# Kernel optimization log

Hardware: AMD Instinct MI355X
Metric: run time of the kernel (lower is better)

Reference implementation:

```python
import jax, jax.numpy as jnp
import numpy as np
from jax import lax

T, B, D, H, L = 256, 64, 512, 1024, 2


def _lstm_params(key):
    k = 1.0 / np.sqrt(H)
    params = {}
    in_dims = [D] + [H] * (L - 1)
    for l in range(L):
        key, k1, k2, k3, k4 = jax.random.split(key, 5)
        params[f"W_ih{l}"] = jax.random.uniform(k1, (4 * H, in_dims[l]), jnp.float32, -k, k)
        params[f"W_hh{l}"] = jax.random.uniform(k2, (4 * H, H), jnp.float32, -k, k)
        params[f"b_ih{l}"] = jax.random.uniform(k3, (4 * H,), jnp.float32, -k, k)
        params[f"b_hh{l}"] = jax.random.uniform(k4, (4 * H,), jnp.float32, -k, k)
    return params


def setup_inputs() -> dict:
    key = jax.random.key(0)
    k_in, k_rst, k_p = jax.random.split(key, 3)
    inp = {
        "input": jax.random.normal(k_in, (T, B, D), jnp.float32),
        "reset": jax.random.randint(k_rst, (T, B), 0, 2, jnp.int32),
        "h0": jnp.zeros((B, L, H), jnp.float32),
        "c0": jnp.zeros((B, L, H), jnp.float32),
    }
    inp.update(_lstm_params(k_p))
    return inp


def _run(input, reset_f, h0, c0, Wi, Wh, bi, bh):
    # state: [L, B, H]
    h = jnp.transpose(h0, (1, 0, 2))
    c = jnp.transpose(c0, (1, 0, 2))

    def step(carry, xt):
        h, c = carry
        x_t, r_t = xt  # x_t: [B, D], r_t: [B]
        keep = (1.0 - r_t)[None, :, None]  # reset gate zeroes state where reset==1
        h = h * keep
        c = c * keep
        x = x_t
        hs, cs = [], []
        for l in range(L):
            # gate order in torch nn.LSTM: i, f, g, o
            gates = x @ Wi[l].T + bi[l] + h[l] @ Wh[l].T + bh[l]
            i_g, f_g, g_g, o_g = jnp.split(gates, 4, axis=-1)
            c_new = jax.nn.sigmoid(f_g) * c[l] + jax.nn.sigmoid(i_g) * jnp.tanh(g_g)
            h_new = jax.nn.sigmoid(o_g) * jnp.tanh(c_new)
            hs.append(h_new)
            cs.append(c_new)
            x = h_new
        return (jnp.stack(hs), jnp.stack(cs)), x

    (h, c), outputs = lax.scan(step, (h, c), (input, reset_f))
    # back to [B, L, H] as in the torch module's returned state
    return outputs, jnp.transpose(h, (1, 0, 2)), jnp.transpose(c, (1, 0, 2))


def reference(input, reset, h0, c0, W_ih0, W_hh0, b_ih0, b_hh0, W_ih1, W_hh1, b_ih1, b_hh1):
    reset_f = reset.astype(jnp.float32)
    Wi = [W_ih0, W_ih1]
    Wh = [W_hh0, W_hh1]
    bi = [b_ih0, b_ih1]
    bh = [b_hh0, b_hh1]
    outputs, hN, cN = _run(input, reset_f, h0, c0, Wi, Wh, bi, bh)
    return outputs, (hN, cN)
```

## Files before the change

### kernel.cpp

```cpp
#include <hip/hip_runtime.h>

typedef __bf16 bf16x8 __attribute__((ext_vector_type(8)));
typedef float f32x4 __attribute__((ext_vector_type(4)));
typedef unsigned u32x4 __attribute__((ext_vector_type(4)));
typedef unsigned short u16;

constexpr int T = 256, B = 64, D = 512, H = 1024;
constexpr int G4 = 4 * H;
constexpr int NBLK = 256;
constexpr int NTHR = 256;
constexpr int BS = 32;
constexpr int MT = 2;

__device__ __forceinline__ u16 f2bf(float f) {
  unsigned u = __builtin_bit_cast(unsigned, f);
  u += 0x7fffu + ((u >> 16) & 1u);
  return (u16)(u >> 16);
}

__device__ __forceinline__ f32x4 mfma16(bf16x8 a, bf16x8 b, f32x4 c) {
  return __builtin_amdgcn_mfma_f32_16x16x32_bf16(a, b, c, 0, 0, 0);
}

__device__ __forceinline__ float sigm(float x) { return 1.f / (1.f + expf(-x)); }

__device__ __forceinline__ int ldflag(const int* f, int i) {
  return __hip_atomic_load(&f[i], __ATOMIC_RELAXED, __HIP_MEMORY_SCOPE_AGENT);
}

__global__ void cvt_bf16(const float* __restrict__ src, u16* __restrict__ dst, int n4) {
  int i = blockIdx.x * blockDim.x + threadIdx.x;
  int st = gridDim.x * blockDim.x;
  for (; i < n4; i += st) {
    float4 v = reinterpret_cast<const float4*>(src)[i];
    ushort4 o;
    o.x = f2bf(v.x); o.y = f2bf(v.y); o.z = f2bf(v.z); o.w = f2bf(v.w);
    reinterpret_cast<ushort4*>(dst)[i] = o;
  }
}

__global__ void init_state(const float* __restrict__ h0,
                           u16* __restrict__ xs1, u16* __restrict__ h1buf,
                           const float* __restrict__ bih0, const float* __restrict__ bhh0,
                           const float* __restrict__ bih1, const float* __restrict__ bhh1,
                           float* __restrict__ bias0, float* __restrict__ bias1,
                           int* __restrict__ flags) {
  int i = blockIdx.x * blockDim.x + threadIdx.x;
  if (i < NBLK) flags[i] = 0;
  if (i < 2 * B * H) {
    int l = i / (B * H), rem = i % (B * H);
    int b = rem / H, k = rem % H;
    u16 v = f2bf(h0[(size_t)b * 2 * H + (size_t)l * H + k]);
    if (l == 0) xs1[(size_t)b * H + k] = v;
    else        h1buf[(size_t)b * H + k] = v;
  }
  if (i < G4) {
    bias0[i] = bih0[i] + bhh0[i];
    bias1[i] = bih1[i] + bhh1[i];
  }
}

template <int L>
__device__ __forceinline__ void run_layer(
    const u16* __restrict__ xin, const u16* __restrict__ wx, const u16* __restrict__ wh,
    const float* __restrict__ bias, u16* __restrict__ xs1, u16* __restrict__ h1b,
    const float* __restrict__ c0, const int* __restrict__ reset,
    float* __restrict__ out, int* __restrict__ flags, int half, int col0, int lb,
    f32x4* __restrict__ red, unsigned* __restrict__ rbits, float* __restrict__ lbias,
    const int s1mask, const int h1mask, const int full) {
  constexpr int KX   = L ? H : D;
  constexpr int NCX  = KX / 32;
  constexpr int NCXW = NCX / 4;
  constexpr int NHW  = (H / 32) / 4;
  constexpr int NCW  = NCXW + NHW;
  const size_t BH = (size_t)B * H;
  const size_t OUT_HN = (size_t)T * BH;
  const size_t OUT_CN = OUT_HN + 2 * BH;

  const int tid  = threadIdx.x;
  const int ks   = tid >> 6;
  const int lane = tid & 63;
  const int q    = lane >> 4;
  const int ln   = lane & 15;

  for (int t = tid; t < T; t += NTHR) {
    unsigned v = 0;
#pragma unroll 8
    for (int i = 0; i < 32; ++i)
      v |= (unsigned)(reset[t * B + half * BS + i] & 1) << i;
    rbits[t] = v;
  }
  if (tid < 64) lbias[tid] = bias[(tid >> 4) * H + col0 + (tid & 15)];

  u32x4 wreg[4][NCW];
#pragma unroll
  for (int g = 0; g < 4; ++g)
#pragma unroll
    for (int cc = 0; cc < NCW; ++cc) {
      const bool isx = cc < NCXW;
      const int c = isx ? ks * NCXW + cc : ks * NHW + (cc - NCXW);
      const u16* W = isx ? wx : wh;
      const int stride = isx ? KX : H;
      const int kk = c * 32 + q * 8;
      wreg[g][cc] = *reinterpret_cast<const u32x4*>(
          W + (size_t)(g * H + col0 + ln) * stride + kk);
    }
#pragma unroll
  for (int g = 0; g < 4; ++g)
#pragma unroll
    for (int cc = 0; cc < NCW; ++cc)
      asm volatile("" : "+a"(wreg[g][cc]));

  const int b0l = (tid >> 4) * 4;
  const int cl  = col0 + (tid & 15);
  float creg[4] = {0.f, 0.f, 0.f, 0.f};
  if (tid < 128)
#pragma unroll
    for (int r = 0; r < 4; ++r)
      creg[r] = c0[(size_t)(half * BS + b0l + r) * 2 * H + (size_t)L * H + cl];

  __syncthreads();
  float bval[4];
#pragma unroll
  for (int g = 0; g < 4; ++g) bval[g] = lbias[g * 16 + (tid & 15)];

  float hv[4] = {0.f, 0.f, 0.f, 0.f};

  uint4 xf[NCXW][MT];
  auto load_xfrags = [&](const u16* xsrc) {
#pragma unroll
    for (int cc = 0; cc < NCXW; ++cc) {
      const int kk = (ks * NCXW + cc) * 32 + q * 8;
#pragma unroll
      for (int m = 0; m < MT; ++m)
        xf[cc][m] = *reinterpret_cast<const uint4*>(
            xsrc + (size_t)(half * BS + 16 * m + ln) * KX + kk);
    }
  };
  if (full && L == 0) load_xfrags(xin);

  const int gbase = (L * 2 + half) * 64 + ks * 16;
  const int xbase = half * 64 + ks * 16;
  int l0seen = 0;

  for (int s = 0; s <= T; ++s) {
    const bool active = (L == 0) ? (s < T) : (s >= 1);
    const int t = (L == 0) ? s : s - 1;
    if (active) {
      const u16* hsrc = (L == 0) ? xs1 + (size_t)(s & s1mask) * BH
                                 : h1b + (size_t)(t & h1mask) * BH;
      if (full) {
        while (ldflag(flags, gbase + (lane & 15)) < s) __builtin_amdgcn_s_sleep(1);
        asm volatile("" ::: "memory");
      } else {
        for (;;) {
          int a = ldflag(flags, lane),       b = ldflag(flags, 64 + lane);
          int c = ldflag(flags, 128 + lane), d = ldflag(flags, 192 + lane);
          int m1 = a < b ? a : b, m2 = c < d ? c : d;
          if ((m1 < m2 ? m1 : m2) >= s) break;
          __builtin_amdgcn_s_sleep(1);
        }
        __builtin_amdgcn_fence(__ATOMIC_ACQUIRE, "agent");
        asm volatile("" ::: "memory");
        load_xfrags((L == 0) ? xin + (size_t)t * B * D
                             : xs1 + (size_t)(s & s1mask) * BH);
      }

      uint4 hf[NHW][MT];
#pragma unroll
      for (int cc = 0; cc < NHW; ++cc) {
        const int kk = (ks * NHW + cc) * 32 + q * 8;
#pragma unroll
        for (int m = 0; m < MT; ++m)
          hf[cc][m] = *reinterpret_cast<const uint4*>(
              hsrc + (size_t)(half * BS + 16 * m + ln) * H + kk);
      }

      f32x4 acc[4][MT];
#pragma unroll
      for (int g = 0; g < 4; ++g)
#pragma unroll
        for (int m = 0; m < MT; ++m) acc[g][m] = (f32x4){0.f, 0.f, 0.f, 0.f};

#pragma unroll
      for (int cc = 0; cc < NCXW; ++cc)
#pragma unroll
        for (int g = 0; g < 4; ++g)
#pragma unroll
          for (int m = 0; m < MT; ++m)
            acc[g][m] = mfma16(__builtin_bit_cast(bf16x8, xf[cc][m]),
                               __builtin_bit_cast(bf16x8, wreg[g][cc]), acc[g][m]);

      const unsigned rw = rbits[t];
      const int rz0 = (int)((rw >> ln) & 1u);
      const int rz1 = (int)((rw >> (16 + ln)) & 1u);
      const uint4 zz = make_uint4(0u, 0u, 0u, 0u);
#pragma unroll
      for (int cc = 0; cc < NHW; ++cc) {
        const uint4 v0 = rz0 ? zz : hf[cc][0];
        const uint4 v1 = rz1 ? zz : hf[cc][1];
#pragma unroll
        for (int g = 0; g < 4; ++g) {
          acc[g][0] = mfma16(__builtin_bit_cast(bf16x8, v0),
                             __builtin_bit_cast(bf16x8, wreg[g][NCXW + cc]), acc[g][0]);
          acc[g][1] = mfma16(__builtin_bit_cast(bf16x8, v1),
                             __builtin_bit_cast(bf16x8, wreg[g][NCXW + cc]), acc[g][1]);
        }
      }

#pragma unroll
      for (int g = 0; g < 4; ++g)
#pragma unroll
        for (int m = 0; m < MT; ++m)
          red[(g * 4 + ks) * (MT * 64) + m * 64 + lane] = acc[g][m];
      __syncthreads();

      if (tid < 128) {
        f32x4 gate[4];
#pragma unroll
        for (int g = 0; g < 4; ++g) {
          f32x4 sum = red[(g * 4 + 0) * (MT * 64) + tid];
#pragma unroll
          for (int w = 1; w < 4; ++w) sum += red[(g * 4 + w) * (MT * 64) + tid];
          gate[g] = sum + (f32x4){bval[g], bval[g], bval[g], bval[g]};
        }
        const unsigned rstw = rbits[t] >> b0l;
        u16 hb[4];
#pragma unroll
        for (int r = 0; r < 4; ++r) {
          float cp = ((rstw >> r) & 1u) ? 0.f : creg[r];
          float i_ = sigm(gate[0][r]);
          float f_ = sigm(gate[1][r]);
          float g_ = tanhf(gate[2][r]);
          float o_ = sigm(gate[3][r]);
          float cn = fmaf(f_, cp, i_ * g_);
          float hn = o_ * tanhf(cn);
          creg[r] = cn;
          hv[r] = hn;
          hb[r] = f2bf(hn);
        }
        if (s < T) {
          u16* hdst = (L == 0)
              ? xs1 + (size_t)((s + 1) & s1mask) * BH
              : h1b + (size_t)((t + 1) & h1mask) * BH;
#pragma unroll
          for (int r = 0; r < 4; ++r) {
            unsigned own = hb[r];
            unsigned oth = (unsigned)__shfl_xor((int)own, 1);
            unsigned pk = (tid & 1) ? ((oth & 0xffffu) | (own << 16))
                                    : (own | (oth << 16));
            if ((r >> 1) == (tid & 1))
              __hip_atomic_store(
                  reinterpret_cast<unsigned*>(
                      hdst + (size_t)(half * BS + b0l + r) * H + (cl & ~1)),
                  pk, __ATOMIC_RELAXED, __HIP_MEMORY_SCOPE_AGENT);
          }
        }
        if (t == T - 1) {
#pragma unroll
          for (int r = 0; r < 4; ++r) {
            const size_t brow = (size_t)(half * BS + b0l + r);
            __builtin_nontemporal_store(
                hv[r], &out[OUT_HN + brow * 2 * H + (size_t)L * H + cl]);
            __builtin_nontemporal_store(
                creg[r], &out[OUT_CN + brow * 2 * H + (size_t)L * H + cl]);
            if (L == 1)
              __builtin_nontemporal_store(
                  hv[r], &out[(size_t)t * BH + brow * H + cl]);
          }
        }
      }
    }

    if (s < T) {
      __syncthreads();
      if (tid == 0)
        __hip_atomic_store(&flags[lb], s + 1,
                           __ATOMIC_RELAXED, __HIP_MEMORY_SCOPE_AGENT);
      if (L == 1 && active && t < T - 1 && tid < 128) {
#pragma unroll
        for (int r = 0; r < 4; ++r)
          out[(size_t)t * BH + (size_t)(half * BS + b0l + r) * H + cl] = hv[r];
      }
      if (full) {
        if (L == 0) {
          if (s + 1 < T) load_xfrags(xin + (size_t)(s + 1) * B * D);
        } else {
          if (l0seen < s + 1) {
            int fv;
            for (;;) {
              fv = ldflag(flags, xbase + (lane & 15));
              if (__all(fv >= s + 1)) break;
              __builtin_amdgcn_s_sleep(1);
            }
            int mn = fv;
#pragma unroll
            for (int o = 1; o < 64; o <<= 1) mn = min(mn, __shfl_xor(mn, o));
            l0seen = mn;
            asm volatile("" ::: "memory");
          }
          load_xfrags(xs1 + (size_t)((s + 1) & s1mask) * BH);
        }
      }
    }
  }
}

__global__ void __launch_bounds__(NTHR, 1) lstm_seq(
    const u16* __restrict__ xin,
    const u16* __restrict__ wx0, const u16* __restrict__ wh0,
    const u16* __restrict__ wx1, const u16* __restrict__ wh1,
    const float* __restrict__ bias0, const float* __restrict__ bias1,
    u16* __restrict__ xs1, u16* __restrict__ h1b,
    const float* __restrict__ c0, const int* __restrict__ reset,
    float* __restrict__ out, int* __restrict__ flags,
    int s1mask, int h1mask, int full) {
  __shared__ f32x4 red[4 * 4 * MT * 64];
  __shared__ unsigned rbits[T];
  __shared__ float lbias[64];
  const int g    = (blockIdx.x & 7) >> 1;
  const int c    = ((blockIdx.x >> 3) << 1) | (blockIdx.x & 1);
  const int half = g & 1;
  const int col0 = c << 4;
  const int lb   = g * 64 + c;
  if ((g >> 1) == 0)
    run_layer<0>(xin, wx0, wh0, bias0, xs1, h1b, c0, reset, out, flags, half, col0, lb,
                 red, rbits, lbias, s1mask, h1mask, full);
  else
    run_layer<1>(nullptr, wx1, wh1, bias1, xs1, h1b, c0, reset, out, flags, half, col0, lb,
                 red, rbits, lbias, s1mask, h1mask, full);
}

extern "C" void kernel_launch(void* const* d_in, const int* in_sizes, int n_in,
                              void* d_out, int out_size, void* d_ws, size_t ws_size,
                              hipStream_t stream) {
  (void)in_sizes; (void)n_in; (void)out_size;
  const float* input = (const float*)d_in[0];
  const int*   reset = (const int*)d_in[1];
  const float* h0    = (const float*)d_in[2];
  const float* c0    = (const float*)d_in[3];
  const float* Wih0  = (const float*)d_in[4];
  const float* Whh0  = (const float*)d_in[5];
  const float* bih0  = (const float*)d_in[6];
  const float* bhh0  = (const float*)d_in[7];
  const float* Wih1  = (const float*)d_in[8];
  const float* Whh1  = (const float*)d_in[9];
  const float* bih1  = (const float*)d_in[10];
  const float* bhh1  = (const float*)d_in[11];
  float* out = (float*)d_out;
  char* ws = (char*)d_ws;

  const size_t SLOT = (size_t)B * H * 2;
  const size_t FIXED = (size_t)G4 * D * 2 + 3 * (size_t)G4 * H * 2
                     + (size_t)T * B * D * 2
                     + 2 * (size_t)G4 * 4 + 8192;
  const bool full = ws_size >= FIXED + 2 * (size_t)(T + 1) * SLOT + 65536;
  const int d0 = full ? (T + 1) : 4;
  const int d1 = full ? (T + 1) : 2;
  const int s1mask = full ? 511 : 3;
  const int h1mask = full ? 511 : 1;

  size_t off = 0;
  auto alloc = [&](size_t bytes) { size_t o = off; off += (bytes + 255) & ~(size_t)255; return o; };
  u16* wx0 = (u16*)(ws + alloc((size_t)G4 * D * 2));
  u16* wh0 = (u16*)(ws + alloc((size_t)G4 * H * 2));
  u16* wx1 = (u16*)(ws + alloc((size_t)G4 * H * 2));
  u16* wh1 = (u16*)(ws + alloc((size_t)G4 * H * 2));
  u16* xin = (u16*)(ws + alloc((size_t)T * B * D * 2));
  u16* xs1 = (u16*)(ws + alloc((size_t)d0 * SLOT));
  u16* h1b = (u16*)(ws + alloc((size_t)d1 * SLOT));
  float* pb0 = (float*)(ws + alloc((size_t)G4 * 4));
  float* pb1 = (float*)(ws + alloc((size_t)G4 * 4));
  int* flg = (int*)(ws + alloc(1024));

  cvt_bf16<<<1024, 256, 0, stream>>>(Wih0, wx0, G4 * D / 4);
  cvt_bf16<<<1024, 256, 0, stream>>>(Whh0, wh0, G4 * H / 4);
  cvt_bf16<<<1024, 256, 0, stream>>>(Wih1, wx1, G4 * H / 4);
  cvt_bf16<<<1024, 256, 0, stream>>>(Whh1, wh1, G4 * H / 4);
  cvt_bf16<<<2048, 256, 0, stream>>>(input, xin, T * B * D / 4);
  init_state<<<512, 256, 0, stream>>>(h0, xs1, h1b, bih0, bhh0, bih1, bhh1, pb0, pb1, flg);
  lstm_seq<<<NBLK, NTHR, 0, stream>>>(xin, wx0, wh0, wx1, wh1, pb0, pb1,
                                      xs1, h1b, c0, reset, out, flg,
                                      s1mask, h1mask, full ? 1 : 0);
}
```

Before: 1.817 ms.

## Replace per-step flag barriers with data-valued polling on zero-initialized state slots

In the full-buffer path, producers no longer publish per-step flags. Consumers load hidden-state data directly and spin only on 32-bit words that are still zero, using nonzero sentinels (packed zero values are forced to 1) to mark readiness. The reduction buffer is double-buffered so the trailing __syncthreads can be dropped, and the state slots are pre-zeroed by extra kernels. This removes a grid-wide flag round trip and a block barrier from the serial recurrence critical path. The cost is extra zeroing traffic, a slight numerical perturbation when a value is exactly zero, and reliance on ordering and visibility of relaxed loads of the data itself.

```diff
diff --git a/kernel.cpp b/kernel.cpp
--- a/kernel.cpp
+++ b/kernel.cpp
@@ -26,6 +26,15 @@
 
 __device__ __forceinline__ int ldflag(const int* f, int i) {
   return __hip_atomic_load(&f[i], __ATOMIC_RELAXED, __HIP_MEMORY_SCOPE_AGENT);
+}
+
+__device__ __forceinline__ unsigned poll_u32(const unsigned* p) {
+  unsigned v = __hip_atomic_load(p, __ATOMIC_RELAXED, __HIP_MEMORY_SCOPE_AGENT);
+  while (v == 0u) {
+    __builtin_amdgcn_s_sleep(1);
+    v = __hip_atomic_load(p, __ATOMIC_RELAXED, __HIP_MEMORY_SCOPE_AGENT);
+  }
+  return v;
 }
 
 __global__ void cvt_bf16(const float* __restrict__ src, u16* __restrict__ dst, int n4) {
@@ -37,6 +46,13 @@
     o.x = f2bf(v.x); o.y = f2bf(v.y); o.z = f2bf(v.z); o.w = f2bf(v.w);
     reinterpret_cast<ushort4*>(dst)[i] = o;
   }
+}
+
+__global__ void zero_u4(uint4* __restrict__ dst, int n) {
+  int i = blockIdx.x * blockDim.x + threadIdx.x;
+  int st = gridDim.x * blockDim.x;
+  const uint4 z = make_uint4(0u, 0u, 0u, 0u);
+  for (; i < n; i += st) dst[i] = z;
 }
 
 __global__ void init_state(const float* __restrict__ h0,
@@ -51,6 +67,7 @@
     int l = i / (B * H), rem = i % (B * H);
     int b = rem / H, k = rem % H;
     u16 v = f2bf(h0[(size_t)b * 2 * H + (size_t)l * H + k]);
+    if (v == 0) v = 1;
     if (l == 0) xs1[(size_t)b * H + k] = v;
     else        h1buf[(size_t)b * H + k] = v;
   }
@@ -139,9 +156,7 @@
   };
   if (full && L == 0) load_xfrags(xin);
 
-  const int gbase = (L * 2 + half) * 64 + ks * 16;
-  const int xbase = half * 64 + ks * 16;
-  int l0seen = 0;
+  const u16* xsrc_prev = xs1;
 
   for (int s = 0; s <= T; ++s) {
     const bool active = (L == 0) ? (s < T) : (s >= 1);
@@ -149,9 +164,41 @@
     if (active) {
       const u16* hsrc = (L == 0) ? xs1 + (size_t)(s & s1mask) * BH
                                  : h1b + (size_t)(t & h1mask) * BH;
+      uint4 hf[NHW][MT];
+
       if (full) {
-        while (ldflag(flags, gbase + (lane & 15)) < s) __builtin_amdgcn_s_sleep(1);
-        asm volatile("" ::: "memory");
+#pragma unroll
+        for (int cc = 0; cc < NHW; ++cc) {
+          const int kk = (ks * NHW + cc) * 32 + q * 8;
+#pragma unroll
+          for (int m = 0; m < MT; ++m)
+            hf[cc][m] = *reinterpret_cast<const uint4*>(
+                hsrc + (size_t)(half * BS + 16 * m + ln) * H + kk);
+        }
+        if (L == 1) {
+          unsigned mn = 0xffffffffu;
+#pragma unroll
+          for (int cc = 0; cc < NCXW; ++cc)
+#pragma unroll
+            for (int m = 0; m < MT; ++m) {
+              mn = min(mn, min(min(xf[cc][m].x, xf[cc][m].y),
+                               min(xf[cc][m].z, xf[cc][m].w)));
+            }
+          if (mn == 0u) {
+#pragma unroll
+            for (int cc = 0; cc < NCXW; ++cc)
+#pragma unroll
+              for (int m = 0; m < MT; ++m) {
+                const unsigned* p = reinterpret_cast<const unsigned*>(
+                    xsrc_prev + (size_t)(half * BS + 16 * m + ln) * KX +
+                    (ks * NCXW + cc) * 32 + q * 8);
+                if (xf[cc][m].x == 0u) xf[cc][m].x = poll_u32(p + 0);
+                if (xf[cc][m].y == 0u) xf[cc][m].y = poll_u32(p + 1);
+                if (xf[cc][m].z == 0u) xf[cc][m].z = poll_u32(p + 2);
+                if (xf[cc][m].w == 0u) xf[cc][m].w = poll_u32(p + 3);
+              }
+          }
+        }
       } else {
         for (;;) {
           int a = ldflag(flags, lane),       b = ldflag(flags, 64 + lane);
@@ -164,16 +211,14 @@
         asm volatile("" ::: "memory");
         load_xfrags((L == 0) ? xin + (size_t)t * B * D
                              : xs1 + (size_t)(s & s1mask) * BH);
-      }
-
-      uint4 hf[NHW][MT];
-#pragma unroll
-      for (int cc = 0; cc < NHW; ++cc) {
-        const int kk = (ks * NHW + cc) * 32 + q * 8;
-#pragma unroll
-        for (int m = 0; m < MT; ++m)
-          hf[cc][m] = *reinterpret_cast<const uint4*>(
-              hsrc + (size_t)(half * BS + 16 * m + ln) * H + kk);
+#pragma unroll
+        for (int cc = 0; cc < NHW; ++cc) {
+          const int kk = (ks * NHW + cc) * 32 + q * 8;
+#pragma unroll
+          for (int m = 0; m < MT; ++m)
+            hf[cc][m] = *reinterpret_cast<const uint4*>(
+                hsrc + (size_t)(half * BS + 16 * m + ln) * H + kk);
+        }
       }
 
       f32x4 acc[4][MT];
@@ -190,6 +235,31 @@
           for (int m = 0; m < MT; ++m)
             acc[g][m] = mfma16(__builtin_bit_cast(bf16x8, xf[cc][m]),
                                __builtin_bit_cast(bf16x8, wreg[g][cc]), acc[g][m]);
+
+      if (full) {
+        unsigned mn = 0xffffffffu;
+#pragma unroll
+        for (int cc = 0; cc < NHW; ++cc)
+#pragma unroll
+          for (int m = 0; m < MT; ++m) {
+            mn = min(mn, min(min(hf[cc][m].x, hf[cc][m].y),
+                             min(hf[cc][m].z, hf[cc][m].w)));
+          }
+        if (mn == 0u) {
+#pragma unroll
+          for (int cc = 0; cc < NHW; ++cc)
+#pragma unroll
+            for (int m = 0; m < MT; ++m) {
+              const unsigned* p = reinterpret_cast<const unsigned*>(
+                  hsrc + (size_t)(half * BS + 16 * m + ln) * H +
+                  (ks * NHW + cc) * 32 + q * 8);
+              if (hf[cc][m].x == 0u) hf[cc][m].x = poll_u32(p + 0);
+              if (hf[cc][m].y == 0u) hf[cc][m].y = poll_u32(p + 1);
+              if (hf[cc][m].z == 0u) hf[cc][m].z = poll_u32(p + 2);
+              if (hf[cc][m].w == 0u) hf[cc][m].w = poll_u32(p + 3);
+            }
+        }
+      }
 
       const unsigned rw = rbits[t];
       const int rz0 = (int)((rw >> ln) & 1u);
@@ -208,20 +278,21 @@
         }
       }
 
+      f32x4* rbuf = red + (size_t)(s & 1) * (16 * 128);
 #pragma unroll
       for (int g = 0; g < 4; ++g)
 #pragma unroll
         for (int m = 0; m < MT; ++m)
-          red[(g * 4 + ks) * (MT * 64) + m * 64 + lane] = acc[g][m];
+          rbuf[(g * 4 + ks) * 128 + m * 64 + lane] = acc[g][m];
       __syncthreads();
 
       if (tid < 128) {
         f32x4 gate[4];
 #pragma unroll
         for (int g = 0; g < 4; ++g) {
-          f32x4 sum = red[(g * 4 + 0) * (MT * 64) + tid];
-#pragma unroll
-          for (int w = 1; w < 4; ++w) sum += red[(g * 4 + w) * (MT * 64) + tid];
+          f32x4 sum = rbuf[(g * 4 + 0) * 128 + tid];
+#pragma unroll
+          for (int w = 1; w < 4; ++w) sum += rbuf[(g * 4 + w) * 128 + tid];
           gate[g] = sum + (f32x4){bval[g], bval[g], bval[g], bval[g]};
         }
         const unsigned rstw = rbits[t] >> b0l;
@@ -249,6 +320,7 @@
             unsigned oth = (unsigned)__shfl_xor((int)own, 1);
             unsigned pk = (tid & 1) ? ((oth & 0xffffu) | (own << 16))
                                     : (own | (oth << 16));
+            if (pk == 0u) pk = 1u;
             if ((r >> 1) == (tid & 1))
               __hip_atomic_store(
                   reinterpret_cast<unsigned*>(
@@ -273,10 +345,6 @@
     }
 
     if (s < T) {
-      __syncthreads();
-      if (tid == 0)
-        __hip_atomic_store(&flags[lb], s + 1,
-                           __ATOMIC_RELAXED, __HIP_MEMORY_SCOPE_AGENT);
       if (L == 1 && active && t < T - 1 && tid < 128) {
 #pragma unroll
         for (int r = 0; r < 4; ++r)
@@ -286,21 +354,14 @@
         if (L == 0) {
           if (s + 1 < T) load_xfrags(xin + (size_t)(s + 1) * B * D);
         } else {
-          if (l0seen < s + 1) {
-            int fv;
-            for (;;) {
-              fv = ldflag(flags, xbase + (lane & 15));
-              if (__all(fv >= s + 1)) break;
-              __builtin_amdgcn_s_sleep(1);
-            }
-            int mn = fv;
-#pragma unroll
-            for (int o = 1; o < 64; o <<= 1) mn = min(mn, __shfl_xor(mn, o));
-            l0seen = mn;
-            asm volatile("" ::: "memory");
-          }
-          load_xfrags(xs1 + (size_t)((s + 1) & s1mask) * BH);
-        }
+          xsrc_prev = xs1 + (size_t)((s + 1) & s1mask) * BH;
+          load_xfrags(xsrc_prev);
+        }
+      } else {
+        __syncthreads();
+        if (tid == 0)
+          __hip_atomic_store(&flags[lb], s + 1,
+                             __ATOMIC_RELAXED, __HIP_MEMORY_SCOPE_AGENT);
       }
     }
   }
@@ -315,7 +376,7 @@
     const float* __restrict__ c0, const int* __restrict__ reset,
     float* __restrict__ out, int* __restrict__ flags,
     int s1mask, int h1mask, int full) {
-  __shared__ f32x4 red[4 * 4 * MT * 64];
+  __shared__ f32x4 red[2 * 16 * 128];
   __shared__ unsigned rbits[T];
   __shared__ float lbias[64];
   const int g    = (blockIdx.x & 7) >> 1;
@@ -378,6 +439,11 @@
   cvt_bf16<<<1024, 256, 0, stream>>>(Wih1, wx1, G4 * H / 4);
   cvt_bf16<<<1024, 256, 0, stream>>>(Whh1, wh1, G4 * H / 4);
   cvt_bf16<<<2048, 256, 0, stream>>>(input, xin, T * B * D / 4);
+  if (full) {
+    const int n4 = (int)((size_t)T * B * H * 2 / 16);
+    zero_u4<<<2048, 256, 0, stream>>>((uint4*)(xs1 + (size_t)B * H), n4);
+    zero_u4<<<2048, 256, 0, stream>>>((uint4*)(h1b + (size_t)B * H), n4);
+  }
   init_state<<<512, 256, 0, stream>>>(h0, xs1, h1b, bih0, bhh0, bih1, bhh1, pb0, pb1, flg);
   lstm_seq<<<NBLK, NTHR, 0, stream>>>(xin, wx0, wh0, wx1, wh1, pb0, pb1,
                                       xs1, h1b, c0, reset, out, flg,
```

Result: slower. 4.296 ms (+136.4%).
